# Kernel optimization log

Measured on AMD Instinct MI355X. Metric: run time of the kernel, lower is better.

## Reference

```python
import math
import jax, jax.numpy as jnp
import numpy as np

B, S, D = 8, 1024, 1024
H, DK = 16, 64
NUM_BUCKETS, MAX_DIST = 32, 128
LN_EPS = 1e-6


def _relative_position_bucket(relative_position, num_buckets=NUM_BUCKETS, max_distance=MAX_DIST):
    # bidirectional (encoder) variant of T5 bucketing
    nb = num_buckets // 2
    rel_buckets = (relative_position > 0).astype(jnp.int32) * nb
    rp = jnp.abs(relative_position)
    max_exact = nb // 2
    is_small = rp < max_exact
    rp_large = max_exact + (
        jnp.log(jnp.maximum(rp, 1).astype(jnp.float32) / max_exact)
        / math.log(max_distance / max_exact)
        * (nb - max_exact)
    ).astype(jnp.int32)
    rp_large = jnp.minimum(rp_large, nb - 1)
    return rel_buckets + jnp.where(is_small, rp, rp_large)


def compute_bias(rel_bias, q_len, k_len):
    ctx = jnp.arange(q_len)[:, None]
    mem = jnp.arange(k_len)[None, :]
    buckets = _relative_position_bucket(mem - ctx)        # [q,k]
    values = rel_bias[buckets]                             # [q,k,H]
    return jnp.transpose(values, (2, 0, 1))[None]          # [1,H,q,k]


def switch_layer_norm(x, w, eps=LN_EPS):
    # T5-style: no mean subtraction, no bias
    var = jnp.mean(jnp.square(x.astype(jnp.float32)), axis=-1, keepdims=True)
    return w * (x * jax.lax.rsqrt(var + eps)).astype(x.dtype)


def setup_inputs() -> dict:
    key = jax.random.key(0)
    ks = jax.random.split(key, 6)
    scale = 1.0 / math.sqrt(D)
    return {
        "hidden_states": jax.random.normal(ks[0], (B, S, D), jnp.float32),
        "ln_weight": jnp.ones((D,), jnp.float32),
        "wq": jax.random.normal(ks[1], (D, H * DK), jnp.float32) * scale,
        "wk": jax.random.normal(ks[2], (D, H * DK), jnp.float32) * scale,
        "wv": jax.random.normal(ks[3], (D, H * DK), jnp.float32) * scale,
        "wo": jax.random.normal(ks[4], (H * DK, D), jnp.float32) * scale,
        "rel_bias": jax.random.normal(ks[5], (NUM_BUCKETS, H), jnp.float32),
    }


def reference(hidden_states, ln_weight, wq, wk, wv, wo, rel_bias):
    b, s, d = hidden_states.shape
    normed = switch_layer_norm(hidden_states, ln_weight)
    # projections -> [B,H,S,DK]; T5 applies NO 1/sqrt(dk) scaling
    q = (normed @ wq).reshape(b, s, H, DK).transpose(0, 2, 1, 3)
    k = (normed @ wk).reshape(b, s, H, DK).transpose(0, 2, 1, 3)
    v = (normed @ wv).reshape(b, s, H, DK).transpose(0, 2, 1, 3)
    scores = jnp.einsum("bhqd,bhkd->bhqk", q, k)
    scores = scores + compute_bias(rel_bias, s, s)
    attn = jax.nn.softmax(scores, axis=-1)
    ctx = jnp.einsum("bhqk,bhkd->bhqd", attn, v)
    ctx = ctx.transpose(0, 2, 1, 3).reshape(b, s, H * DK)
    attn_out = ctx @ wo
    return hidden_states + attn_out  # residual of SwitchLayerSelfAttention (dropout=0)
```

## Files before the change

kernel.cpp:

```cpp
#include <hip/hip_runtime.h>

typedef unsigned short u16;
typedef unsigned int u32;
typedef unsigned long long u64;
typedef __attribute__((ext_vector_type(8))) short bf16x8;
typedef __attribute__((ext_vector_type(4))) float f32x4;

__device__ __forceinline__ float bf2f(u16 u) {
  union { u32 i; float f; } c; c.i = ((u32)u) << 16; return c.f;
}
__device__ __forceinline__ u16 f2bf(float f) {
  union { float f; u32 i; } c; c.f = f;
  u32 i = c.i;
  return (u16)((i + 0x7fffu + ((i >> 16) & 1u)) >> 16);
}
__device__ __forceinline__ u32 pkbf(float a, float b) {
  union { float f; u32 i; } ca, cb; ca.f = a; cb.f = b;
  return __builtin_amdgcn_perm(cb.i + 0x8000u, ca.i + 0x8000u, 0x07060302u);
}
__device__ __forceinline__ void async16(const void* g, void* l) {
  __builtin_amdgcn_global_load_lds((const __attribute__((address_space(1))) void*)g,
                                   (__attribute__((address_space(3))) void*)l, 16, 0, 0);
}

__global__ __launch_bounds__(256) void detect_kernel(const u32* __restrict__ X,
                                                     int* __restrict__ flag) {
  __shared__ int part[4];
  const int tid = threadIdx.x, lane = tid & 63, wave = tid >> 6;
  int votes = 0;
  for (int i = tid; i < 4096; i += 256) {
    const u32 u = X[i];
    union { u32 i; float f; } c; c.i = u;
    const float a = fabsf(c.f);
    if (u == 0u || (a > 1e-6f && a < 1e6f)) votes++;
  }
  #pragma unroll
  for (int off = 32; off >= 1; off >>= 1) votes += __shfl_xor(votes, off);
  if (lane == 0) part[wave] = votes;
  __syncthreads();
  if (tid == 0) {
    const int tot = part[0] + part[1] + part[2] + part[3];
    *flag = (tot >= 2048) ? 0 : 1;
  }
}

__global__ __launch_bounds__(256) void prep_kernel(
    const void* __restrict__ W0, const void* __restrict__ W1, const void* __restrict__ W2,
    const void* __restrict__ W3, u16* __restrict__ T0, u16* __restrict__ T1,
    u16* __restrict__ T2, u16* __restrict__ T3, const void* __restrict__ rel_bias,
    float* __restrict__ Tb, const int* __restrict__ flagp) {
  const int f32m = (*flagp == 0);
  const int z = blockIdx.z;
  if (z == 4) {
    const int flat = blockIdx.y * 16 + blockIdx.x;
    const int idx = flat * 256 + threadIdx.x;
    if (idx >= 16 * 2047) return;
    const int h = idx / 2047;
    const int d = idx % 2047 - 1023;
    const int rb = (d > 0) ? 16 : 0;
    const int rp = d < 0 ? -d : d;
    int val;
    if (rp < 8) {
      val = rp;
    } else {
      float t = (logf((float)rp * 0.125f) / 2.772588722239781f) * 8.0f;
      val = 8 + (int)t;
      if (val > 15) val = 15;
    }
    const int bi = (rb + val) * 16 + h;
    Tb[idx] = f32m ? ((const float*)rel_bias)[bi] : bf2f(((const u16*)rel_bias)[bi]);
    return;
  }
  const void* W = (z == 0) ? W0 : (z == 1) ? W1 : (z == 2) ? W2 : W3;
  u16* WT = (z == 0) ? T0 : (z == 1) ? T1 : (z == 2) ? T2 : T3;
  __shared__ u16 t[64][65];
  const int tid = threadIdx.x;
  const int tx = tid & 63, ty = tid >> 6;
  const int n0 = blockIdx.x * 64, k0 = blockIdx.y * 64;
  #pragma unroll
  for (int r = ty; r < 64; r += 4) {
    const size_t idx = (size_t)(k0 + r) * 1024 + n0 + tx;
    t[r][tx] = f32m ? f2bf(((const float*)W)[idx]) : ((const u16*)W)[idx];
  }
  __syncthreads();
  #pragma unroll
  for (int r = ty; r < 64; r += 4) WT[(size_t)(n0 + r) * 1024 + k0 + tx] = t[tx][r];
}

__global__ __launch_bounds__(256) void rmsnorm_kernel(const void* __restrict__ X,
                                                      const void* __restrict__ W,
                                                      u16* __restrict__ Out,
                                                      const int* __restrict__ flagp) {
  const int f32m = (*flagp == 0);
  __shared__ float part[4];
  const int tid = threadIdx.x, lane = tid & 63, wave = tid >> 6;
  const size_t row = blockIdx.x;
  const int c = tid * 4;
  float x0, x1, x2, x3, w0f, w1f, w2f, w3f;
  if (f32m) {
    const float4 xx = *(const float4*)((const float*)X + row * 1024 + c);
    x0 = xx.x; x1 = xx.y; x2 = xx.z; x3 = xx.w;
    const float4 ww = *(const float4*)((const float*)W + c);
    w0f = ww.x; w1f = ww.y; w2f = ww.z; w3f = ww.w;
  } else {
    const u32* px = (const u32*)((const u16*)X + row * 1024 + c);
    const u32 a0 = px[0], a1 = px[1];
    x0 = bf2f((u16)a0); x1 = bf2f((u16)(a0 >> 16));
    x2 = bf2f((u16)a1); x3 = bf2f((u16)(a1 >> 16));
    const u32* pw = (const u32*)((const u16*)W + c);
    const u32 b0 = pw[0], b1 = pw[1];
    w0f = bf2f((u16)b0); w1f = bf2f((u16)(b0 >> 16));
    w2f = bf2f((u16)b1); w3f = bf2f((u16)(b1 >> 16));
  }
  float ss = x0 * x0 + x1 * x1 + x2 * x2 + x3 * x3;
  #pragma unroll
  for (int off = 32; off >= 1; off >>= 1) ss += __shfl_xor(ss, off);
  if (lane == 0) part[wave] = ss;
  __syncthreads();
  const float tot = part[0] + part[1] + part[2] + part[3];
  const float scale = rsqrtf(tot * (1.0f / 1024.0f) + 1e-6f);
  const u16 o0 = f2bf(x0 * scale * w0f);
  const u16 o1 = f2bf(x1 * scale * w1f);
  const u16 o2 = f2bf(x2 * scale * w2f);
  const u16 o3 = f2bf(x3 * scale * w3f);
  u32* po = (u32*)(Out + row * 1024 + c);
  po[0] = (u32)o0 | ((u32)o1 << 16);
  po[1] = (u32)o2 | ((u32)o3 << 16);
}

template <int S0>
__device__ __forceinline__ void stage3(u16* lds, const u16* __restrict__ A,
                                       const u16* __restrict__ B, int m0, int n0,
                                       int kt, int w, int lane) {
  const int ko8 = ((lane & 7) ^ ((lane >> 3) & 7)) * 8;
  const int rl = lane >> 3;
  #pragma unroll
  for (int s = S0; s < S0 + 3; ++s) {
    const int cw = s * 8 + w;
    const int r = cw * 8 + rl;
    u16* ldst = lds + cw * 512;
    if (s < 4)
      async16(A + (size_t)(m0 + r) * 1024 + kt + ko8, ldst);
    else
      async16(B + (size_t)(n0 + r - 256) * 1024 + kt + ko8, ldst);
  }
}

template <bool SWAP>
__device__ __forceinline__ void gemm256_core(const u16* __restrict__ A,
                                             const u16* __restrict__ WT,
                                             u16 (*buf)[24576], f32x4 (&acc)[4][4],
                                             int m0, int n0, int lane, int w) {
  const int wr = w >> 1, wc = w & 1;
  const int l15 = lane & 15;
  const int ko0 = (((lane >> 4) + 0) ^ (lane & 7)) * 8;
  const int ko1 = (((lane >> 4) + 4) ^ (lane & 7)) * 8;
  const int arow = (wr * 64 + l15) * 64;
  const int brow = 16384 + (wc * 64 + l15) * 64;

  stage3<0>(buf[0], A, WT, m0, n0, 0, w, lane);
  stage3<3>(buf[0], A, WT, m0, n0, 0, w, lane);
  stage3<0>(buf[1], A, WT, m0, n0, 64, w, lane);
  stage3<3>(buf[1], A, WT, m0, n0, 64, w, lane);
  __asm__ volatile("s_waitcnt vmcnt(6)" ::: "memory");
  __builtin_amdgcn_s_barrier();
  __asm__ volatile("" ::: "memory");

  int sl = 0, sn = 2;
  #pragma unroll 1
  for (int t = 0; t < 16; ++t) {
    const u16* bc = buf[sl];
    u16* bn = buf[sn];
    const int kt2 = (t + 2) * 64;
    bf16x8 af[4][2], bfr[2][2];
    #pragma unroll
    for (int i = 0; i < 4; ++i) {
      af[i][0] = *(const bf16x8*)(bc + arow + i * 1024 + ko0);
      af[i][1] = *(const bf16x8*)(bc + arow + i * 1024 + ko1);
    }
    #pragma unroll
    for (int j = 0; j < 2; ++j) {
      bfr[j][0] = *(const bf16x8*)(bc + brow + j * 1024 + ko0);
      bfr[j][1] = *(const bf16x8*)(bc + brow + j * 1024 + ko1);
    }
    if (t < 14) stage3<0>(bn, A, WT, m0, n0, kt2, w, lane);
    __builtin_amdgcn_s_barrier();
    __asm__ volatile("s_waitcnt lgkmcnt(0)" ::: "memory");
    __builtin_amdgcn_s_setprio(1);
    #pragma unroll
    for (int i = 0; i < 4; ++i)
      #pragma unroll
      for (int j = 0; j < 2; ++j) {
        if (SWAP) {
          acc[i][j] = __builtin_amdgcn_mfma_f32_16x16x32_bf16(bfr[j][0], af[i][0], acc[i][j], 0, 0, 0);
          acc[i][j] = __builtin_amdgcn_mfma_f32_16x16x32_bf16(bfr[j][1], af[i][1], acc[i][j], 0, 0, 0);
        } else {
          acc[i][j] = __builtin_amdgcn_mfma_f32_16x16x32_bf16(af[i][0], bfr[j][0], acc[i][j], 0, 0, 0);
          acc[i][j] = __builtin_amdgcn_mfma_f32_16x16x32_bf16(af[i][1], bfr[j][1], acc[i][j], 0, 0, 0);
        }
      }
    __builtin_amdgcn_s_setprio(0);
    __builtin_amdgcn_s_barrier();
    __asm__ volatile("" ::: "memory");
    #pragma unroll
    for (int j = 0; j < 2; ++j) {
      bfr[j][0] = *(const bf16x8*)(bc + brow + (j + 2) * 1024 + ko0);
      bfr[j][1] = *(const bf16x8*)(bc + brow + (j + 2) * 1024 + ko1);
    }
    if (t < 14) stage3<3>(bn, A, WT, m0, n0, kt2, w, lane);
    __builtin_amdgcn_s_barrier();
    __asm__ volatile("s_waitcnt lgkmcnt(0)" ::: "memory");
    __builtin_amdgcn_s_setprio(1);
    #pragma unroll
    for (int i = 0; i < 4; ++i)
      #pragma unroll
      for (int j = 0; j < 2; ++j) {
        if (SWAP) {
          acc[i][j + 2] = __builtin_amdgcn_mfma_f32_16x16x32_bf16(bfr[j][0], af[i][0], acc[i][j + 2], 0, 0, 0);
          acc[i][j + 2] = __builtin_amdgcn_mfma_f32_16x16x32_bf16(bfr[j][1], af[i][1], acc[i][j + 2], 0, 0, 0);
        } else {
          acc[i][j + 2] = __builtin_amdgcn_mfma_f32_16x16x32_bf16(af[i][0], bfr[j][0], acc[i][j + 2], 0, 0, 0);
          acc[i][j + 2] = __builtin_amdgcn_mfma_f32_16x16x32_bf16(af[i][1], bfr[j][1], acc[i][j + 2], 0, 0, 0);
        }
      }
    __builtin_amdgcn_s_setprio(0);
    if (t < 14)
      __asm__ volatile("s_waitcnt vmcnt(6)" ::: "memory");
    else
      __asm__ volatile("s_waitcnt vmcnt(0)" ::: "memory");
    __builtin_amdgcn_s_barrier();
    __asm__ volatile("" ::: "memory");
    sl = (sl == 2) ? 0 : sl + 1;
    sn = (sn == 2) ? 0 : sn + 1;
  }
}

__global__ __launch_bounds__(512, 2) void qkv_gemm256_kernel(
    const u16* __restrict__ A, const u16* __restrict__ WT,
    u16* __restrict__ Qo, u16* __restrict__ Ko, u16* __restrict__ VTo) {
  __shared__ __align__(16) u16 buf[3][24576];
  const int tid = threadIdx.x, lane = tid & 63, w = tid >> 6;
  const int id = blockIdx.x;
  const int xcd = id & 7;
  const int t0 = id >> 3;
  const int nb = t0 % 24;
  const int mhi = t0 / 24;
  const int m0 = (mhi * 8 + xcd) * 256;
  const int n0 = nb * 128;
  const int z = nb >> 3;

  f32x4 acc[4][4];
  const f32x4 zero = {0.f, 0.f, 0.f, 0.f};
  #pragma unroll
  for (int i = 0; i < 4; ++i)
    #pragma unroll
    for (int j = 0; j < 4; ++j) acc[i][j] = zero;

  const int wr = w >> 1, wc = w & 1;
  const int cq = lane & 15, quad = lane >> 4;
  const int nbase = (n0 & 1023) + wc * 64;

  if (z == 2) {
    gemm256_core<false>(A, WT, buf, acc, m0, n0, lane, w);
    #pragma unroll
    for (int i = 0; i < 4; ++i) {
      const int s = m0 + wr * 64 + i * 16 + quad * 4;
      const int b = s >> 10, s0 = s & 1023;
      #pragma unroll
      for (int j = 0; j < 4; ++j) {
        const int n = nbase + j * 16 + cq;
        const int hh = n >> 6, dk = n & 63;
        const u64 pk = (u64)f2bf(acc[i][j][0]) | ((u64)f2bf(acc[i][j][1]) << 16) |
                       ((u64)f2bf(acc[i][j][2]) << 32) | ((u64)f2bf(acc[i][j][3]) << 48);
        *(u64*)(VTo + (((size_t)(b * 16 + hh)) * 64 + dk) * 1024 + s0) = pk;
      }
    }
  } else {
    gemm256_core<true>(A, WT, buf, acc, m0, n0, lane, w);
    u16* Out = (z == 0) ? Qo : Ko;
    #pragma unroll
    for (int i = 0; i < 4; ++i) {
      const int s = m0 + wr * 64 + i * 16 + cq;
      const int b = s >> 10, ss = s & 1023;
      #pragma unroll
      for (int j = 0; j < 4; ++j) {
        const int n = nbase + j * 16 + quad * 4;
        const int hh = n >> 6, dk = n & 63;
        const u64 pk = (u64)f2bf(acc[i][j][0]) | ((u64)f2bf(acc[i][j][1]) << 16) |
                       ((u64)f2bf(acc[i][j][2]) << 32) | ((u64)f2bf(acc[i][j][3]) << 48);
        *(u64*)(Out + (((size_t)(b * 16 + hh)) * 1024 + ss) * 64 + dk) = pk;
      }
    }
  }
}

__global__ __launch_bounds__(512, 2) void out_gemm256_kernel(
    const u16* __restrict__ A, const u16* __restrict__ BT, const void* __restrict__ Res,
    void* __restrict__ Out, const int* __restrict__ flagp) {
  const int f32m = (*flagp == 0);
  __shared__ __align__(16) u16 buf[3][24576];
  const int tid = threadIdx.x, lane = tid & 63, w = tid >> 6;
  const int id = blockIdx.x;
  const int xcd = id & 7;
  const int t0 = id >> 3;
  const int nb = t0 & 7;
  const int mhi = t0 >> 3;
  const int m0 = (mhi * 8 + xcd) * 256;
  const int n0 = nb * 128;

  f32x4 acc[4][4];
  const f32x4 zero = {0.f, 0.f, 0.f, 0.f};
  #pragma unroll
  for (int i = 0; i < 4; ++i)
    #pragma unroll
    for (int j = 0; j < 4; ++j) acc[i][j] = zero;

  gemm256_core<true>(A, BT, buf, acc, m0, n0, lane, w);

  const int wr = w >> 1, wc = w & 1;
  const int cq = lane & 15, quad = lane >> 4;
  #pragma unroll
  for (int i = 0; i < 4; ++i) {
    const int s = m0 + wr * 64 + i * 16 + cq;
    #pragma unroll
    for (int j = 0; j < 4; ++j) {
      const int n = n0 + wc * 64 + j * 16 + quad * 4;
      const size_t idx = (size_t)s * 1024 + n;
      if (f32m) {
        const float4 rr = *(const float4*)((const float*)Res + idx);
        float4 oo;
        oo.x = rr.x + acc[i][j][0]; oo.y = rr.y + acc[i][j][1];
        oo.z = rr.z + acc[i][j][2]; oo.w = rr.w + acc[i][j][3];
        *(float4*)((float*)Out + idx) = oo;
      } else {
        const u64 rr = *(const u64*)((const u16*)Res + idx);
        const u64 pk =
            (u64)f2bf(bf2f((u16)rr) + acc[i][j][0]) |
            ((u64)f2bf(bf2f((u16)(rr >> 16)) + acc[i][j][1]) << 16) |
            ((u64)f2bf(bf2f((u16)(rr >> 32)) + acc[i][j][2]) << 32) |
            ((u64)f2bf(bf2f((u16)(rr >> 48)) + acc[i][j][3]) << 48);
        *(u64*)((u16*)Out + idx) = pk;
      }
    }
  }
}

__global__ __launch_bounds__(256, 4) void attn_kernel(
    const u16* __restrict__ Q, const u16* __restrict__ K, const u16* __restrict__ VT,
    const float* __restrict__ Tb, u16* __restrict__ ctx) {
  __shared__ __align__(16) u16 Ks[3][4096];
  __shared__ __align__(16) u16 Ps[4][2048];
  __shared__ __align__(16) float Tbs[1152];

  const int tid = threadIdx.x, lane = tid & 63, w = tid >> 6;
  const int c = lane & 15, quad = lane >> 4;
  const int id = blockIdx.x;
  const int bh = id & 127, qc = id >> 7;
  const int b = bh >> 4, h = bh & 15;
  const int q0 = qc * 128;
  const int qw = q0 + w * 32;
  const u16* Kg = K + (size_t)bh * 1024 * 64;
  const u16* Vg = VT + (size_t)bh * 64 * 1024;
  const float* Th = Tb + h * 2047;
  u16* PsW = &Ps[w][0];

  #pragma unroll
  for (int i = tid; i < 1152; i += 256) Tbs[i] = Th[896 - q0 + i];

  bf16x8 qf[2][2];
  {
    const u16* Qg = Q + ((size_t)bh * 1024 + qw) * 64;
    #pragma unroll
    for (int nt = 0; nt < 2; ++nt)
      #pragma unroll
      for (int half = 0; half < 2; ++half)
        qf[nt][half] = *(const bf16x8*)(Qg + (size_t)(nt * 16 + c) * 64 + half * 32 + quad * 8);
  }

  f32x4 oacc[4][2];
  const f32x4 zero = {0.f, 0.f, 0.f, 0.f};
  #pragma unroll
  for (int i = 0; i < 4; ++i)
    #pragma unroll
    for (int j = 0; j < 2; ++j) oacc[i][j] = zero;
  float rsum[2] = {0.f, 0.f};

  const u16* Ksrc = Kg + (size_t)(w * 16 + c) * 64 + quad * 8;
  const u16* Vp = Vg + (size_t)c * 1024 + quad * 8;

  #pragma unroll
  for (int i = 0; i < 2; ++i) async16(Ksrc + i * 32, &Ks[0][(w * 2 + i) * 512]);
  #pragma unroll
  for (int i = 0; i < 2; ++i) async16(Ksrc + (size_t)64 * 64 + i * 32, &Ks[1][(w * 2 + i) * 512]);
  __syncthreads();

  #pragma unroll 1
  for (int kt = 0; kt < 16; ++kt) {
    const int k0 = kt * 64;
    const u16* Kc = &Ks[kt % 3][0];
    __asm__ volatile("s_waitcnt vmcnt(2)" ::: "memory");
    __builtin_amdgcn_s_barrier();
    __asm__ volatile("" ::: "memory");
    bf16x8 vf[4][2];
    #pragma unroll
    for (int dt = 0; dt < 4; ++dt)
      #pragma unroll
      for (int i = 0; i < 2; ++i)
        vf[dt][i] = *(const bf16x8*)(Vp + (size_t)dt * 16384 + k0 + i * 32);
    __asm__ volatile("" ::: "memory");
    if (kt < 14) {
      const int kn = kt + 2;
      #pragma unroll
      for (int i = 0; i < 2; ++i)
        async16(Ksrc + (size_t)(kn * 64) * 64 + i * 32, &Ks[kn % 3][(w * 2 + i) * 512]);
    }
    __asm__ volatile("" ::: "memory");
    f32x4 sc[4][2];
    const int jb = k0 + quad * 4 - c + 127 - 32 * w;
    #pragma unroll
    for (int mt = 0; mt < 4; ++mt)
      #pragma unroll
      for (int nt = 0; nt < 2; ++nt) {
        const float* tp = Tbs + jb + mt * 16 - nt * 16;
        sc[mt][nt][0] = tp[0]; sc[mt][nt][1] = tp[1]; sc[mt][nt][2] = tp[2]; sc[mt][nt][3] = tp[3];
      }
    #pragma unroll
    for (int mt = 0; mt < 4; ++mt) {
      const bf16x8 kf0 = *(const bf16x8*)(Kc + (mt * 2 + 0) * 512 + lane * 8);
      const bf16x8 kf1 = *(const bf16x8*)(Kc + (mt * 2 + 1) * 512 + lane * 8);
      #pragma unroll
      for (int nt = 0; nt < 2; ++nt) {
        sc[mt][nt] = __builtin_amdgcn_mfma_f32_16x16x32_bf16(kf0, qf[nt][0], sc[mt][nt], 0, 0, 0);
        sc[mt][nt] = __builtin_amdgcn_mfma_f32_16x16x32_bf16(kf1, qf[nt][1], sc[mt][nt], 0, 0, 0);
      }
    }
    #pragma unroll
    for (int mt = 0; mt < 4; ++mt)
      #pragma unroll
      for (int nt = 0; nt < 2; ++nt) {
        const float p0 = __expf(sc[mt][nt][0]), p1 = __expf(sc[mt][nt][1]);
        const float p2 = __expf(sc[mt][nt][2]), p3 = __expf(sc[mt][nt][3]);
        rsum[nt] += (p0 + p1) + (p2 + p3);
        const u32 lo = pkbf(p0, p1), hi = pkbf(p2, p3);
        const u64 pk = (u64)lo | ((u64)hi << 32);
        const int ch = (mt * 2 + (quad >> 1)) ^ (c & 7);
        *(u64*)(PsW + (nt * 16 + c) * 64 + ch * 8 + (quad & 1) * 4) = pk;
      }
    __asm__ volatile("s_waitcnt lgkmcnt(0)" ::: "memory");
    bf16x8 pf[2][2];
    #pragma unroll
    for (int nt = 0; nt < 2; ++nt)
      #pragma unroll
      for (int kk = 0; kk < 2; ++kk) {
        const int ch = (kk * 4 + quad) ^ (c & 7);
        pf[nt][kk] = *(const bf16x8*)(PsW + (nt * 16 + c) * 64 + ch * 8);
      }
    if (kt < 14)
      __asm__ volatile("s_waitcnt vmcnt(2)" ::: "memory");
    else
      __asm__ volatile("s_waitcnt vmcnt(0)" ::: "memory");
    __builtin_amdgcn_s_setprio(1);
    #pragma unroll
    for (int dt = 0; dt < 4; ++dt)
      #pragma unroll
      for (int nt = 0; nt < 2; ++nt) {
        oacc[dt][nt] = __builtin_amdgcn_mfma_f32_16x16x32_bf16(vf[dt][0], pf[nt][0], oacc[dt][nt], 0, 0, 0);
        oacc[dt][nt] = __builtin_amdgcn_mfma_f32_16x16x32_bf16(vf[dt][1], pf[nt][1], oacc[dt][nt], 0, 0, 0);
      }
    __builtin_amdgcn_s_setprio(0);
  }

  #pragma unroll
  for (int nt = 0; nt < 2; ++nt) {
    rsum[nt] += __shfl_xor(rsum[nt], 16);
    rsum[nt] += __shfl_xor(rsum[nt], 32);
  }

  #pragma unroll
  for (int nt = 0; nt < 2; ++nt) {
    const float inv = 1.0f / rsum[nt];
    const int q = qw + nt * 16 + c;
    #pragma unroll
    for (int dt = 0; dt < 4; ++dt) {
      const u64 pk = (u64)f2bf(oacc[dt][nt][0] * inv) | ((u64)f2bf(oacc[dt][nt][1] * inv) << 16) |
                     ((u64)f2bf(oacc[dt][nt][2] * inv) << 32) | ((u64)f2bf(oacc[dt][nt][3] * inv) << 48);
      *(u64*)(ctx + (((size_t)b * 1024 + q) * 16 + h) * 64 + dt * 16 + quad * 4) = pk;
    }
  }
}

extern "C" void kernel_launch(void* const* d_in, const int* in_sizes, int n_in,
                              void* d_out, int out_size, void* d_ws, size_t ws_size,
                              hipStream_t stream) {
  const void* hidden = d_in[0];
  const void* lnw = d_in[1];
  const void* wq = d_in[2];
  const void* wk = d_in[3];
  const void* wv = d_in[4];
  const void* wo = d_in[5];
  const void* relb = d_in[6];
  char* ws = (char*)d_ws;

  u16* normed = (u16*)(ws);
  u16* Qb = (u16*)(ws + ((size_t)16 << 20));
  u16* Kb = (u16*)(ws + ((size_t)32 << 20));
  u16* VTb = (u16*)(ws + ((size_t)48 << 20));
  u16* wtq = (u16*)(ws + ((size_t)64 << 20));
  u16* wtk = (u16*)(ws + ((size_t)64 << 20) + (2 << 20));
  u16* wtv = (u16*)(ws + ((size_t)64 << 20) + (4 << 20));
  u16* wto = (u16*)(ws + ((size_t)64 << 20) + (6 << 20));
  float* Tb = (float*)(ws + ((size_t)64 << 20) + (8 << 20));
  int* flag = (int*)(ws + ((size_t)64 << 20) + (9 << 20));

  dim3 b256(256);
  detect_kernel<<<dim3(1), b256, 0, stream>>>((const u32*)hidden, flag);
  prep_kernel<<<dim3(16, 16, 5), b256, 0, stream>>>(wq, wk, wv, wo, wtq, wtk, wtv, wto,
                                                    relb, Tb, flag);
  rmsnorm_kernel<<<dim3(8192), b256, 0, stream>>>(hidden, lnw, normed, flag);
  qkv_gemm256_kernel<<<dim3(768), dim3(512), 0, stream>>>(normed, wtq, Qb, Kb, VTb);
  attn_kernel<<<dim3(1024), b256, 0, stream>>>(Qb, Kb, VTb, Tb, normed);
  out_gemm256_kernel<<<dim3(256), dim3(512), 0, stream>>>(normed, wto, hidden, d_out, flag);
}
```

Measured before the change: 287.5 us.

## Double query tile per attention block and stage V through LDS

The attention kernel now runs 512 threads and 256 queries per block, so each K/V tile loaded from global memory serves twice as many queries. V is loaded asynchronously into a double-buffered LDS tile next to K, where before each wave read it straight from global into registers. The three-stage K ring becomes a two-stage buffer with a full vmcnt(0) wait and block barrier every iteration, and the setprio hint is removed. This cuts global traffic but may expose load latency and lower occupancy because of the larger LDS footprint and block size.

Result: faster. 257.8 us (-10.4%).

```diff
diff --git a/kernel.cpp b/kernel.cpp
--- a/kernel.cpp
+++ b/kernel.cpp
@@ -345,27 +345,27 @@
   }
 }
 
-__global__ __launch_bounds__(256, 4) void attn_kernel(
+__global__ __launch_bounds__(512, 4) void attn_kernel(
     const u16* __restrict__ Q, const u16* __restrict__ K, const u16* __restrict__ VT,
     const float* __restrict__ Tb, u16* __restrict__ ctx) {
-  __shared__ __align__(16) u16 Ks[3][4096];
-  __shared__ __align__(16) u16 Ps[4][2048];
-  __shared__ __align__(16) float Tbs[1152];
+  __shared__ __align__(16) u16 Ks[2][4096];
+  __shared__ __align__(16) u16 Vs[2][4096];
+  __shared__ __align__(16) u16 Ps[8][2048];
+  __shared__ __align__(16) float Tbs[1280];
 
   const int tid = threadIdx.x, lane = tid & 63, w = tid >> 6;
   const int c = lane & 15, quad = lane >> 4;
   const int id = blockIdx.x;
   const int bh = id & 127, qc = id >> 7;
   const int b = bh >> 4, h = bh & 15;
-  const int q0 = qc * 128;
+  const int q0 = qc * 256;
   const int qw = q0 + w * 32;
   const u16* Kg = K + (size_t)bh * 1024 * 64;
   const u16* Vg = VT + (size_t)bh * 64 * 1024;
   const float* Th = Tb + h * 2047;
   u16* PsW = &Ps[w][0];
 
-  #pragma unroll
-  for (int i = tid; i < 1152; i += 256) Tbs[i] = Th[896 - q0 + i];
+  for (int i = tid; i < 1280; i += 512) Tbs[i] = Th[768 - q0 + i];
 
   bf16x8 qf[2][2];
   {
@@ -385,38 +385,25 @@
     for (int j = 0; j < 2; ++j) oacc[i][j] = zero;
   float rsum[2] = {0.f, 0.f};
 
-  const u16* Ksrc = Kg + (size_t)(w * 16 + c) * 64 + quad * 8;
-  const u16* Vp = Vg + (size_t)c * 1024 + quad * 8;
-
-  #pragma unroll
-  for (int i = 0; i < 2; ++i) async16(Ksrc + i * 32, &Ks[0][(w * 2 + i) * 512]);
-  #pragma unroll
-  for (int i = 0; i < 2; ++i) async16(Ksrc + (size_t)64 * 64 + i * 32, &Ks[1][(w * 2 + i) * 512]);
-  __syncthreads();
+  const u16* Ksrc = Kg + (size_t)((w >> 1) * 16 + c) * 64 + (w & 1) * 32 + quad * 8;
+  const u16* Vsrc = Vg + (size_t)((w >> 1) * 16 + c) * 1024 + (w & 1) * 32 + quad * 8;
+
+  async16(Ksrc, &Ks[0][w * 512]);
+  async16(Vsrc, &Vs[0][w * 512]);
 
   #pragma unroll 1
   for (int kt = 0; kt < 16; ++kt) {
+    const int cur = kt & 1;
     const int k0 = kt * 64;
-    const u16* Kc = &Ks[kt % 3][0];
-    __asm__ volatile("s_waitcnt vmcnt(2)" ::: "memory");
-    __builtin_amdgcn_s_barrier();
-    __asm__ volatile("" ::: "memory");
-    bf16x8 vf[4][2];
-    #pragma unroll
-    for (int dt = 0; dt < 4; ++dt)
-      #pragma unroll
-      for (int i = 0; i < 2; ++i)
-        vf[dt][i] = *(const bf16x8*)(Vp + (size_t)dt * 16384 + k0 + i * 32);
-    __asm__ volatile("" ::: "memory");
-    if (kt < 14) {
-      const int kn = kt + 2;
-      #pragma unroll
-      for (int i = 0; i < 2; ++i)
-        async16(Ksrc + (size_t)(kn * 64) * 64 + i * 32, &Ks[kn % 3][(w * 2 + i) * 512]);
-    }
-    __asm__ volatile("" ::: "memory");
+    __asm__ volatile("s_waitcnt vmcnt(0)" ::: "memory");
+    __syncthreads();
+    if (kt < 15) {
+      const int k1 = (kt + 1) * 64;
+      async16(Ksrc + (size_t)k1 * 64, &Ks[1 - cur][w * 512]);
+      async16(Vsrc + k1, &Vs[1 - cur][w * 512]);
+    }
     f32x4 sc[4][2];
-    const int jb = k0 + quad * 4 - c + 127 - 32 * w;
+    const int jb = k0 + quad * 4 - c + 255 - 32 * w;
     #pragma unroll
     for (int mt = 0; mt < 4; ++mt)
       #pragma unroll
@@ -424,6 +411,7 @@
         const float* tp = Tbs + jb + mt * 16 - nt * 16;
         sc[mt][nt][0] = tp[0]; sc[mt][nt][1] = tp[1]; sc[mt][nt][2] = tp[2]; sc[mt][nt][3] = tp[3];
       }
+    const u16* Kc = &Ks[cur][0];
     #pragma unroll
     for (int mt = 0; mt < 4; ++mt) {
       const bf16x8 kf0 = *(const bf16x8*)(Kc + (mt * 2 + 0) * 512 + lane * 8);
@@ -447,6 +435,7 @@
         *(u64*)(PsW + (nt * 16 + c) * 64 + ch * 8 + (quad & 1) * 4) = pk;
       }
     __asm__ volatile("s_waitcnt lgkmcnt(0)" ::: "memory");
+    const u16* Vc = &Vs[cur][0];
     bf16x8 pf[2][2];
     #pragma unroll
     for (int nt = 0; nt < 2; ++nt)
@@ -455,19 +444,16 @@
         const int ch = (kk * 4 + quad) ^ (c & 7);
         pf[nt][kk] = *(const bf16x8*)(PsW + (nt * 16 + c) * 64 + ch * 8);
       }
-    if (kt < 14)
-      __asm__ volatile("s_waitcnt vmcnt(2)" ::: "memory");
-    else
-      __asm__ volatile("s_waitcnt vmcnt(0)" ::: "memory");
-    __builtin_amdgcn_s_setprio(1);
-    #pragma unroll
-    for (int dt = 0; dt < 4; ++dt)
+    #pragma unroll
+    for (int dt = 0; dt < 4; ++dt) {
+      const bf16x8 vf0 = *(const bf16x8*)(Vc + (dt * 2 + 0) * 512 + lane * 8);
+      const bf16x8 vf1 = *(const bf16x8*)(Vc + (dt * 2 + 1) * 512 + lane * 8);
       #pragma unroll
       for (int nt = 0; nt < 2; ++nt) {
-        oacc[dt][nt] = __builtin_amdgcn_mfma_f32_16x16x32_bf16(vf[dt][0], pf[nt][0], oacc[dt][nt], 0, 0, 0);
-        oacc[dt][nt] = __builtin_amdgcn_mfma_f32_16x16x32_bf16(vf[dt][1], pf[nt][1], oacc[dt][nt], 0, 0, 0);
-      }
-    __builtin_amdgcn_s_setprio(0);
+        oacc[dt][nt] = __builtin_amdgcn_mfma_f32_16x16x32_bf16(vf0, pf[nt][0], oacc[dt][nt], 0, 0, 0);
+        oacc[dt][nt] = __builtin_amdgcn_mfma_f32_16x16x32_bf16(vf1, pf[nt][1], oacc[dt][nt], 0, 0, 0);
+      }
+    }
   }
 
   #pragma unroll
@@ -518,6 +504,6 @@
                                                     relb, Tb, flag);
   rmsnorm_kernel<<<dim3(8192), b256, 0, stream>>>(hidden, lnw, normed, flag);
   qkv_gemm256_kernel<<<dim3(768), dim3(512), 0, stream>>>(normed, wtq, Qb, Kb, VTb);
-  attn_kernel<<<dim3(1024), b256, 0, stream>>>(Qb, Kb, VTb, Tb, normed);
+  attn_kernel<<<dim3(512), dim3(512), 0, stream>>>(Qb, Kb, VTb, Tb, normed);
   out_gemm256_kernel<<<dim3(256), dim3(512), 0, stream>>>(normed, wto, hidden, d_out, flag);
 }
```
